# Optimization experiments

Hardware: AMD Instinct MI355X
Metric: run time of the kernel (lower is better)

## Reference

```python
import jax, jax.numpy as jnp
import numpy as np
from jax import lax

EPOCHS = 3
D_IN, D_OUT = 20, 18
_BN_EPS = 1e-5
_RECT_EPS = 1e-4


def _sym(a):
    return 0.5 * (a + jnp.swapaxes(a, -1, -2))


def _logm(a):
    s, u = jnp.linalg.eigh(_sym(a))
    return jnp.einsum('...ij,...j,...kj->...ik', u, jnp.log(s), u)


def _expm(a):
    s, u = jnp.linalg.eigh(_sym(a))
    return jnp.einsum('...ij,...j,...kj->...ik', u, jnp.exp(s), u)


def _rectify(a):
    # SPDRectified: clamp eigenvalues at epsilon
    s, u = jnp.linalg.eigh(_sym(a))
    s = jnp.maximum(s, _RECT_EPS)
    return jnp.einsum('...ij,...j,...kj->...ik', u, s, u)


def _bn(x, g, b):
    # training-mode BatchNorm2d (biased variance, as torch uses for normalization)
    m = x.mean(axis=(0, 2, 3), keepdims=True)
    v = x.var(axis=(0, 2, 3), keepdims=True)
    return (x - m) * lax.rsqrt(v + _BN_EPS) * g[None, :, None, None] + b[None, :, None, None]


def _patch_lens(n, epochs):
    base = n // epochs
    lens = [base] * epochs
    for i in range(n - base * epochs):
        lens[i] += 1
    return lens


def _forward(x, conv1_w, conv1_b, bn1_g, bn1_b, conv2_w, conv2_b, bn2_g, bn2_b,
             Wq, Wk, Wv, lin_w, lin_b):
    B = x.shape[0]
    # conv1: Conv2d(1, 22, (22, 1)) -- full contraction over the 22 EEG channels
    h = jnp.einsum('oh,bht->bot', conv1_w, x[:, 0]) + conv1_b[None, :, None]
    h = _bn(h[:, :, None, :], bn1_g, bn1_b)  # (B,22,1,T)
    # conv2: Conv2d(22, 20, (1, 12), padding=(0, 6)) -> time length T+1
    h = lax.conv_general_dilated(h, conv2_w, (1, 1), [(0, 0), (6, 6)],
                                 dimension_numbers=('NCHW', 'OIHW', 'NCHW'))
    h = h + conv2_b[None, :, None, None]
    h = _bn(h, bn2_g, bn2_b)
    sig = h[:, :, 0, :]  # (B, 20, T+1)
    # E2R: split time axis into EPOCHS patches, trace-normalized covariance per patch
    covs, off = [], 0
    eye = jnp.eye(D_IN, dtype=x.dtype)
    for L in _patch_lens(sig.shape[-1], EPOCHS):
        seg = sig[:, :, off:off + L]
        off += L
        seg = seg - seg.mean(axis=-1, keepdims=True)
        c = seg @ jnp.swapaxes(seg, -1, -2) / (L - 1)
        c = c / jnp.trace(c, axis1=-2, axis2=-1)[:, None, None]
        covs.append(c + 1e-5 * eye)
    cov = jnp.stack(covs, axis=1)  # (B, EPOCHS, 20, 20)
    # SPDTransform (bilinear congruence W^T X W) for Q, K, V
    Q = jnp.einsum('ia,bmij,jc->bmac', Wq, cov, Wq)
    K = jnp.einsum('ia,bmij,jc->bmac', Wk, cov, Wk)
    V = jnp.einsum('ia,bmij,jc->bmac', Wv, cov, Wv)
    logQ, logK, logV = _logm(Q), _logm(K), _logm(V)
    # log-Euclidean distance: sum of singular values of D D^T == ||D||_F^2
    # energy[b, i, j] = || logK[b,i] - logQ[b,j] ||_F^2 (matches the repeat/expand layout)
    diff = logK[:, :, None] - logQ[:, None, :]  # (B, m, m, d, d)
    energy = jnp.sum(diff * diff, axis=(-1, -2))  # (B, m, m)
    f = 1.0 / (1.0 + jnp.log1p(energy))
    prob = jax.nn.softmax(f, axis=-2)      # softmax over dim=-2 (the K index)
    prob = jnp.swapaxes(prob, -1, -2)      # permute(0, 2, 1)
    # LogEuclideanMean: weighted mean in log domain, then matrix exp
    mean_log = jnp.einsum('bpi,bikl->bpkl', prob, logV)
    out = _expm(mean_log)
    out = _rectify(out)
    tang = _logm(out)
    ri, ci = np.triu_indices(D_OUT)
    feat = tang[:, :, ri, ci].reshape(B, -1)  # (B, EPOCHS * 171)
    return feat @ lin_w.T + lin_b


def setup_inputs():
    key = jax.random.key(0)
    ks = jax.random.split(key, 16)
    B, C, T = 1024, 22, 438
    f32 = jnp.float32
    return {
        'x': jax.random.normal(ks[0], (B, 1, C, T), f32),
        'conv1_w': 0.1 * jax.random.normal(ks[1], (22, 22), f32),
        'conv1_b': 0.1 * jax.random.normal(ks[2], (22,), f32),
        'bn1_g': 1.0 + 0.1 * jax.random.normal(ks[3], (22,), f32),
        'bn1_b': 0.1 * jax.random.normal(ks[4], (22,), f32),
        'conv2_w': 0.05 * jax.random.normal(ks[5], (20, 22, 1, 12), f32),
        'conv2_b': 0.1 * jax.random.normal(ks[6], (20,), f32),
        'bn2_g': 1.0 + 0.1 * jax.random.normal(ks[7], (20,), f32),
        'bn2_b': 0.1 * jax.random.normal(ks[8], (20,), f32),
        'Wq': jnp.linalg.qr(jax.random.normal(ks[9], (20, 18), f32))[0],
        'Wk': jnp.linalg.qr(jax.random.normal(ks[10], (20, 18), f32))[0],
        'Wv': jnp.linalg.qr(jax.random.normal(ks[11], (20, 18), f32))[0],
        'lin_w': 0.05 * jax.random.normal(ks[12], (4, 9 * 19 * EPOCHS), f32),
        'lin_b': jnp.zeros((4,), f32),
    }


def reference(x, conv1_w, conv1_b, bn1_g, bn1_b, conv2_w, conv2_b, bn2_g, bn2_b,
              Wq, Wk, Wv, lin_w, lin_b):
    return _forward(x, conv1_w, conv1_b, bn1_g, bn1_b, conv2_w, conv2_b,
                    bn2_g, bn2_b, Wq, Wk, Wv, lin_w, lin_b)
```

## Files before the change

### kernel.cpp

```cpp
#include <hip/hip_runtime.h>
#include <cmath>

#define B_ 1024
#define CIN_ 22
#define T1_ 438
#define COUT_ 20
#define T2_ 439

#define OFF_S 0
#define OFF_M 32
#define OFF_SUM2 576
#define OFF_SSQ2 608
#define OFF_A2 640
#define OFF_ACC_END 704
#define OFF_C 1024
#define OFF_LQ (OFF_C + B_*3*400)
#define OFF_LK (OFF_LQ + B_*3*324)
#define OFF_LV (OFF_LK + B_*3*324)
#define OFF_WEFF (OFF_LV + B_*3*324)
#define OFF_BPRE (OFF_WEFF + 5280)

__global__ __launch_bounds__(256) void k_zero(float* ws){
  for(int i=threadIdx.x; i<OFF_ACC_END; i+=256) ws[i]=0.f;
}

__global__ __launch_bounds__(256) void k_moment(const float* __restrict__ x, float* __restrict__ ws){
  __shared__ float xs[CIN_][440];
  int b=blockIdx.x;
  const float* xb = x + (size_t)b*CIN_*T1_;
  for(int i=threadIdx.x;i<CIN_*T1_;i+=256){
    int h=i/T1_, t=i-h*T1_;
    xs[h][t]=xb[i];
  }
  if(threadIdx.x<CIN_){ xs[threadIdx.x][438]=0.f; xs[threadIdx.x][439]=0.f; }
  __syncthreads();
  for(int tgt=threadIdx.x; tgt<275; tgt+=256){
    if(tgt<253){
      int r=tgt, i=0;
      while(true){ int c=CIN_-i; if(r<c) break; r-=c; i++; }
      int j=i+r;
      const float4* ri=(const float4*)&xs[i][0];
      const float4* rj=(const float4*)&xs[j][0];
      float acc=0.f;
      for(int t=0;t<110;t++){
        float4 a=ri[t], bb=rj[t];
        acc += a.x*bb.x + a.y*bb.y + a.z*bb.z + a.w*bb.w;
      }
      atomicAdd(&ws[OFF_M + i*CIN_ + j], acc);
    } else {
      int c=tgt-253;
      const float4* rc=(const float4*)&xs[c][0];
      float acc=0.f;
      for(int t=0;t<110;t++){
        float4 a=rc[t];
        acc += a.x + a.y + a.z + a.w;
      }
      atomicAdd(&ws[OFF_S + c], acc);
    }
  }
}

__global__ __launch_bounds__(256) void k_prep(const float* __restrict__ w1, const float* __restrict__ cb1,
                                              const float* __restrict__ g1, const float* __restrict__ bb1,
                                              const float* __restrict__ w2, float* __restrict__ ws){
  __shared__ float a1s[CIN_], e1s[CIN_];
  int tid=threadIdx.x;
  if(tid<CIN_){
    int c=tid;
    const double N = (double)B_*T1_;
    double wS=0.0, wMw=0.0;
    for(int h=0;h<CIN_;h++) wS += (double)w1[c*CIN_+h]*(double)ws[OFF_S+h];
    for(int h=0;h<CIN_;h++){
      for(int h2=0;h2<CIN_;h2++){
        int i=h<h2?h:h2, j=h<h2?h2:h;
        wMw += (double)w1[c*CIN_+h]*(double)w1[c*CIN_+h2]*(double)ws[OFF_M+i*CIN_+j];
      }
    }
    double bc=cb1[c];
    double mean=wS/N+bc;
    double ex2=(wMw+2.0*bc*wS)/N+bc*bc;
    double var=ex2-mean*mean;
    double a1=(double)g1[c]/sqrt(var+1e-5);
    double d1=(double)bb1[c]-mean*a1;
    a1s[c]=(float)a1;
    e1s[c]=(float)(a1*bc+d1);
  }
  __syncthreads();
  for(int idx=tid; idx<5280; idx+=256){
    int o=idx/264, r=idx-o*264, h=r/12, k=r-h*12;
    float s=0.f;
    for(int i=0;i<CIN_;i++) s += w2[(o*CIN_+i)*12+k]*a1s[i]*w1[i*CIN_+h];
    ws[OFF_WEFF+idx]=s;
  }
  if(tid<COUT_){
    float pre=0.f;
    ws[OFF_BPRE+tid*13+0]=0.f;
    for(int k=0;k<12;k++){
      float wb=0.f;
      for(int i=0;i<CIN_;i++) wb += w2[(tid*CIN_+i)*12+k]*e1s[i];
      pre += wb;
      ws[OFF_BPRE+tid*13+k+1]=pre;
    }
  }
}

__global__ __launch_bounds__(256) void k_cov(const float* __restrict__ x,
                                             float* __restrict__ ws){
  __shared__ float Wl[5280];
  __shared__ float preL[COUT_][13];
  __shared__ float xs[CIN_][168];
  __shared__ float h2w[COUT_][156];
  __shared__ float pmu[COUT_];
  int b=blockIdx.x, tid=threadIdx.x;
  for(int i=tid;i<5280;i+=256) Wl[i]=ws[OFF_WEFF+i];
  for(int i=tid;i<260;i+=256) ((float*)preL)[i]=ws[OFF_BPRE+i];
  int pi=0,pj=0;
  if(tid<210){ int r=tid,i=0; while(true){int c=COUT_-i; if(r<c)break; r-=c; i++;} pi=i; pj=i+r; }
  int sc = tid-210;
  float ac1=0.f, ac2=0.f;
  const float* xb = x + (size_t)b*CIN_*T1_;
  int o = tid/12, cch = tid-12*o;
  int t0 = cch*13;
  for(int p=0;p<3;p++){
    const int off = (p==0)?0:((p==1)?147:293);
    const int L = (p==0)?147:146;
    __syncthreads();
    for(int idx=tid; idx<CIN_*168; idx+=256){
      int h=idx/168, c2=idx-h*168;
      int gxt = off-6+c2;
      xs[h][c2] = (c2<167 && gxt>=0 && gxt<T1_) ? xb[h*T1_+gxt] : 0.f;
    }
    __syncthreads();
    if(tid<240){
      float acc[13];
      #pragma unroll
      for(int j=0;j<13;j++){
        int gt = off+t0+j;
        int kmin = 6-gt; kmin = kmin<0?0:kmin;
        int kmax = 443-gt; kmax = kmax>11?11:kmax;
        acc[j] = (kmax>=kmin)? preL[o][kmax+1]-preL[o][kmin] : 0.f;
      }
      const float* Wo = &Wl[o*264];
      for(int h=0;h<CIN_;h++){
        float xw[24];
        #pragma unroll
        for(int c2=0;c2<24;c2++) xw[c2]=xs[h][t0+c2];
        const float* Wh = Wo + h*12;
        #pragma unroll
        for(int k=0;k<12;k++){
          float w=Wh[k];
          #pragma unroll
          for(int j=0;j<13;j++) acc[j] += w*xw[j+k];
        }
      }
      #pragma unroll
      for(int j=0;j<13;j++) if(t0+j<L) h2w[o][t0+j]=acc[j];
    } else {
      int npad = 156-L;
      for(int z=tid-240; z<COUT_*npad; z+=16){
        int oo=z/npad, c2=z-oo*npad;
        h2w[oo][L+c2]=0.f;
      }
    }
    __syncthreads();
    float s=0.f;
    if(tid<210){
      const float4* ri=(const float4*)&h2w[pi][0];
      const float4* rj=(const float4*)&h2w[pj][0];
      for(int t=0;t<39;t++){
        float4 a=ri[t], bb=rj[t];
        s += a.x*bb.x + a.y*bb.y + a.z*bb.z + a.w*bb.w;
      }
    } else if(sc>=0 && sc<COUT_){
      const float4* rc=(const float4*)&h2w[sc][0];
      float s1=0.f,s2=0.f;
      for(int t=0;t<39;t++){
        float4 a=rc[t];
        s1 += a.x+a.y+a.z+a.w;
        s2 += a.x*a.x+a.y*a.y+a.z*a.z+a.w*a.w;
      }
      ac1+=s1; ac2+=s2; pmu[sc]=s1/(float)L;
    }
    __syncthreads();
    if(tid<210){
      s -= (float)L*pmu[pi]*pmu[pj];
      float* Cb = ws + OFF_C + ((size_t)b*3+p)*400;
      Cb[pi*COUT_+pj]=s; Cb[pj*COUT_+pi]=s;
    }
  }
  if(sc>=0 && sc<COUT_){
    atomicAdd(&ws[OFF_SUM2+sc], ac1);
    atomicAdd(&ws[OFF_SSQ2+sc], ac2);
  }
}

__global__ void k_fin2(const float* __restrict__ g2, float* __restrict__ ws){
  int c=threadIdx.x; if(c>=COUT_) return;
  const double N=(double)B_*T2_;
  double m=ws[OFF_SUM2+c]/N;
  double v=ws[OFF_SSQ2+c]/N - m*m;
  ws[OFF_A2+c]=(float)((double)g2[c]/sqrt(v+1e-5));
}

__device__ __forceinline__ void bl_jacobi18(float own[18], float &dgo,
                                            int l18, int gb, bool act, int maxsweep){
  int self = gb + l18;
  for(int sweep=0; sweep<maxsweep; sweep++){
    { float d0=0.f,d1=0.f;
      #pragma unroll
      for(int k=0;k<18;k+=2){ d0+=own[k]*own[k]; d1+=own[k+1]*own[k+1]; }
      dgo=d0+d1;
    }
    float smax=0.f;
    for(int r=0;r<17;r++){
      int t = 2*r - l18;
      t += (t<0)?17:0;
      t -= (t>=17)?17:0;
      int pa = (l18==17)? r : ((t==l18)?17:t);
      int src = act ? (gb + pa) : self;
      float oth[18];
      #pragma unroll
      for(int k=0;k<18;k++) oth[k]=__shfl(own[k], src);
      float dgx = __shfl(dgo, src);
      float a0=0.f,a1=0.f;
      #pragma unroll
      for(int k=0;k<18;k+=2){ a0+=own[k]*oth[k]; a1+=own[k+1]*oth[k+1]; }
      float apq=a0+a1;
      bool isP = l18 < pa;
      float dgp = isP? dgo : dgx;
      float dgq = isP? dgx : dgo;
      float tau = __fdividef(dgq-dgp, 2.f*apq);
      float tt  = __fdividef(copysignf(1.f,tau), fabsf(tau)+sqrtf(1.f+tau*tau));
      float c   = rsqrtf(1.f+tt*tt);
      float s   = tt*c;
      bool  z   = (apq==0.f) || !act;
      tt=z?0.f:tt; c=z?1.f:c; s=z?0.f:s;
      smax=fmaxf(smax,fabsf(s));
      float sgn = isP ? -s : s;
      #pragma unroll
      for(int k=0;k<18;k++) own[k] = c*own[k] + sgn*oth[k];
      dgo = isP ? (dgp - tt*apq) : (dgq + tt*apq);
    }
    if(__all(smax<3e-3f)) break;
  }
  float d0=0.f,d1=0.f;
  #pragma unroll
  for(int k=0;k<18;k+=2){ d0+=own[k]*own[k]; d1+=own[k+1]*own[k+1]; }
  dgo=d0+d1;
}

__global__ __launch_bounds__(64) void k_eigh3(const float* __restrict__ Wq,
                                              const float* __restrict__ Wk,
                                              const float* __restrict__ Wv,
                                              float* __restrict__ ws){
  __shared__ float S[2933];
  float* Wa  = S;
  float* a2s = S+1080;
  float* Cs  = S+1100;
  float* Tt  = S+1500;
  float* ob  = S+1878;
  float* gl  = S+2850;
  float* trp = S+2904;
  int bp=blockIdx.x, tid=threadIdx.x;
  int g=tid/18, l18=tid-18*g;
  bool act = (g<3);
  int gb = g*18;

  if(tid<20) a2s[tid]=ws[OFF_A2+tid];
  __syncthreads();
  for(int i=tid;i<1080;i+=64){
    int m=i/360, r=i-m*360, row=r/18;
    const float* W=(m==0)?Wq:((m==1)?Wk:Wv);
    Wa[i]=W[r]*a2s[row];
  }
  const float* Cb=ws+OFF_C+(size_t)bp*400;
  for(int i=tid;i<400;i+=64) Cs[i]=Cb[i];
  __syncthreads();
  if(tid==0){
    float tr=0.f;
    #pragma unroll
    for(int i=0;i<20;i++) tr += Cs[i*20+i]*a2s[i]*a2s[i];
    trp[0]=tr;
  }
  __syncthreads();
  float tr=trp[0];
  float sh=1e-5f*tr;
  float logtr=logf(tr);
  for(int m=0;m<3;m++){
    const float* Wm=Wa+m*360;
    for(int idx=tid; idx<360; idx+=64){
      int a=idx/20, j=idx-a*20;
      float s=0.f;
      for(int i=0;i<20;i++) s += Wm[i*18+a]*Cs[i*20+j];
      Tt[a*21+j]=s;
    }
    __syncthreads();
    for(int idx=tid; idx<324; idx+=64){
      int a=idx/18, c=idx-a*18;
      float s=0.f;
      for(int j=0;j<20;j++) s += Tt[a*21+j]*Wm[j*18+c];
      ob[m*324+idx]=s;
    }
    __syncthreads();
  }
  float own[18], dgo=0.f;
  if(act){
    const float* Ag=ob+g*324;
    #pragma unroll
    for(int k=0;k<18;k++)
      own[k]=0.5f*(Ag[k*18+l18]+Ag[l18*18+k]) + ((k==l18)?sh:0.f);
  } else {
    #pragma unroll
    for(int k=0;k<18;k++) own[k]=0.f;
  }
  __syncthreads();
  bl_jacobi18(own,dgo,l18,gb,act,8);
  float dp=fmaxf(dgo,1e-30f);
  float gv=__fdividef(0.5f*logf(dp)-logtr, dp);
  float* Mc = Wa;
  if(act){
    #pragma unroll
    for(int k=0;k<18;k++) Mc[g*342 + k*19 + l18]=own[k];
    gl[g*18+l18]=gv;
  }
  __syncthreads();
  if(tid<54){
    int mat=tid/18, i=tid-mat*18;
    float w[18];
    #pragma unroll
    for(int k=0;k<18;k++) w[k]=gl[mat*18+k]*Mc[mat*342+i*19+k];
    for(int j=0;j<18;j++){
      float s=0.f;
      #pragma unroll
      for(int k=0;k<18;k++) s += w[k]*Mc[mat*342+j*19+k];
      ob[mat*324+i*18+j]=s;
    }
  }
  __syncthreads();
  const float4* s4=(const float4*)ob;
  for(int i=tid;i<243;i+=64){
    int mat=i/81, r=i-mat*81;
    float4* dst=(float4*)(ws + ((mat==0)?OFF_LQ:((mat==1)?OFF_LK:OFF_LV)) + (size_t)bp*324);
    dst[r]=s4[i];
  }
}

__global__ __launch_bounds__(64) void k_att2(const float* __restrict__ lw,
                                             const float* __restrict__ lb,
                                             float* __restrict__ ws,
                                             float* __restrict__ out){
  __shared__ float lv[972];
  __shared__ float lqk[1944];
  __shared__ float e9[9];
  __shared__ float prob[9];
  __shared__ float Mc[1026];
  __shared__ float gl[54];
  int b=blockIdx.x, tid=threadIdx.x;
  const float4* LQ4=(const float4*)(ws+OFF_LQ+(size_t)b*972);
  const float4* LK4=(const float4*)(ws+OFF_LK+(size_t)b*972);
  const float4* LV4=(const float4*)(ws+OFF_LV+(size_t)b*972);
  float4* lqk4=(float4*)lqk; float4* lv4=(float4*)lv;
  for(int i=tid;i<243;i+=64){ lqk4[i]=LQ4[i]; lqk4[243+i]=LK4[i]; lv4[i]=LV4[i]; }
  __syncthreads();
  if(tid<36){
    int d=tid>>2, sub=tid&3;
    int ii=d/3, p=d-ii*3;
    const float* kk=lqk+972+ii*324+sub*81;
    const float* qq=lqk+p*324+sub*81;
    float s=0.f;
    for(int el=0;el<81;el++){ float dd=kk[el]-qq[el]; s+=dd*dd; }
    s += __shfl_xor(s,1); s += __shfl_xor(s,2);
    if(sub==0) e9[d]=s;
  }
  __syncthreads();
  if(tid<3){
    int p=tid;
    float f0=1.f/(1.f+log1pf(e9[0+p]));
    float f1=1.f/(1.f+log1pf(e9[3+p]));
    float f2=1.f/(1.f+log1pf(e9[6+p]));
    float mx=fmaxf(f0,fmaxf(f1,f2));
    float x0=expf(f0-mx), x1=expf(f1-mx), x2=expf(f2-mx);
    float inv=1.f/(x0+x1+x2);
    prob[p*3+0]=x0*inv; prob[p*3+1]=x1*inv; prob[p*3+2]=x2*inv;
  }
  __syncthreads();
  float* ml = lqk;
  for(int idx=tid; idx<972; idx+=64){
    int p=idx/324, el=idx-p*324;
    ml[idx]=prob[p*3+0]*lv[el]+prob[p*3+1]*lv[324+el]+prob[p*3+2]*lv[648+el];
  }
  __syncthreads();
  int g=tid/18, l18=tid-18*g;
  bool act=(g<3);
  int gb=g*18;
  float own[18], dgo=0.f;
  if(act){
    const float* Ag=ml+g*324;
    #pragma unroll
    for(int k=0;k<18;k++)
      own[k]=0.5f*(Ag[k*18+l18]+Ag[l18*18+k]) + ((k==l18)?12.f:0.f);
  } else {
    #pragma unroll
    for(int k=0;k<18;k++) own[k]=0.f;
  }
  __syncthreads();
  bl_jacobi18(own,dgo,l18,gb,act,8);
  float lam=sqrtf(fmaxf(dgo,1e-12f));
  float gv=__fdividef(fmaxf(lam-12.f,-9.2103404f), fmaxf(dgo,1e-12f));
  if(act){
    #pragma unroll
    for(int k=0;k<18;k++) Mc[g*342 + k*19 + l18]=own[k];
    gl[g*18+l18]=gv;
  }
  __syncthreads();
  float* feat = lv;
  if(tid<54){
    int mat=tid/18, i=tid-mat*18;
    float w[18];
    #pragma unroll
    for(int k=0;k<18;k++) w[k]=gl[mat*18+k]*Mc[mat*342+i*19+k];
    int base = mat*171 + (i*18 - (i*(i-1))/2) - i;
    for(int j=i;j<18;j++){
      float s=0.f;
      #pragma unroll
      for(int k=0;k<18;k++) s += w[k]*Mc[mat*342+j*19+k];
      feat[base+j]=s;
    }
  }
  __syncthreads();
  int j4 = tid&3, chunk = tid>>2;
  float s=0.f;
  const float* wj = lw + j4*513;
  for(int k=chunk; k<513; k+=16) s += feat[k]*wj[k];
  s += __shfl_xor(s,4); s += __shfl_xor(s,8);
  s += __shfl_xor(s,16); s += __shfl_xor(s,32);
  if(chunk==0) out[b*4+j4] = s + lb[j4];
}

extern "C" void kernel_launch(void* const* d_in, const int* in_sizes, int n_in,
                              void* d_out, int out_size, void* d_ws, size_t ws_size,
                              hipStream_t stream){
  const float* x  =(const float*)d_in[0];
  const float* w1 =(const float*)d_in[1];
  const float* cb1=(const float*)d_in[2];
  const float* g1 =(const float*)d_in[3];
  const float* bb1=(const float*)d_in[4];
  const float* w2 =(const float*)d_in[5];
  const float* g2 =(const float*)d_in[7];
  const float* Wq =(const float*)d_in[9];
  const float* Wk =(const float*)d_in[10];
  const float* Wv =(const float*)d_in[11];
  const float* lw =(const float*)d_in[12];
  const float* lb =(const float*)d_in[13];
  float* ws=(float*)d_ws;
  float* out=(float*)d_out;

  k_zero<<<1,256,0,stream>>>(ws);
  k_moment<<<B_,256,0,stream>>>(x,ws);
  k_prep<<<1,256,0,stream>>>(w1,cb1,g1,bb1,w2,ws);
  k_cov<<<B_,256,0,stream>>>(x,ws);
  k_fin2<<<1,64,0,stream>>>(g2,ws);
  k_eigh3<<<3072,64,0,stream>>>(Wq,Wk,Wv,ws);
  k_att2<<<B_,64,0,stream>>>(lw,lb,ws,out);
}
```

Before: 406.3 us.

## Fuse per-epoch log-eigh and attention kernels into one 192-thread block per sample

Merges the per-(sample,epoch) eigendecomposition kernel and the per-sample attention kernel into one kernel with three wavefronts per sample, one per epoch. The log-mapped Q/K/V matrices stay in shared memory instead of round-tripping through the global workspace, and one launch is removed. The cost is a larger shared-memory footprint per block, and the second-stage Jacobi runs only 18 of 64 lanes in each wave, so occupancy and lane utilisation may drop.

After: 429.1 us, median of 2. +5.6%, slower.

```diff
diff --git a/kernel.cpp b/kernel.cpp
--- a/kernel.cpp
+++ b/kernel.cpp
@@ -14,10 +14,7 @@
 #define OFF_A2 640
 #define OFF_ACC_END 704
 #define OFF_C 1024
-#define OFF_LQ (OFF_C + B_*3*400)
-#define OFF_LK (OFF_LQ + B_*3*324)
-#define OFF_LV (OFF_LK + B_*3*324)
-#define OFF_WEFF (OFF_LV + B_*3*324)
+#define OFF_WEFF (OFF_C + B_*3*400)
 #define OFF_BPRE (OFF_WEFF + 5280)
 
 __global__ __launch_bounds__(256) void k_zero(float* ws){
@@ -249,63 +246,77 @@
   dgo=d0+d1;
 }
 
-__global__ __launch_bounds__(64) void k_eigh3(const float* __restrict__ Wq,
-                                              const float* __restrict__ Wk,
-                                              const float* __restrict__ Wv,
-                                              float* __restrict__ ws){
-  __shared__ float S[2933];
-  float* Wa  = S;
-  float* a2s = S+1080;
-  float* Cs  = S+1100;
-  float* Tt  = S+1500;
-  float* ob  = S+1878;
-  float* gl  = S+2850;
-  float* trp = S+2904;
-  int bp=blockIdx.x, tid=threadIdx.x;
-  int g=tid/18, l18=tid-18*g;
-  bool act = (g<3);
-  int gb = g*18;
-
-  if(tid<20) a2s[tid]=ws[OFF_A2+tid];
-  __syncthreads();
-  for(int i=tid;i<1080;i+=64){
+#define F_A2S 0
+#define F_WA 20
+#define F_CS 1100
+#define F_TT 2300
+#define F_TRS 3434
+#define F_LTR 3437
+#define F_LG 3440
+#define F_E9 6356
+#define F_PROB 6365
+#define F_SC 20
+#define F_GL1 3098
+#define F_ML 20
+#define F_MC2 992
+#define F_GL2 2018
+#define F_FEAT 3440
+
+__global__ __launch_bounds__(192) void k_fused(const float* __restrict__ Wq,
+                                               const float* __restrict__ Wk,
+                                               const float* __restrict__ Wv,
+                                               const float* __restrict__ lw,
+                                               const float* __restrict__ lb,
+                                               float* __restrict__ ws,
+                                               float* __restrict__ out){
+  __shared__ float S[6374];
+  int b=blockIdx.x, tid=threadIdx.x;
+  int w=tid>>6, wl=tid&63;
+  if(tid<20) S[F_A2S+tid]=ws[OFF_A2+tid];
+  __syncthreads();
+  for(int i=tid;i<1080;i+=192){
     int m=i/360, r=i-m*360, row=r/18;
     const float* W=(m==0)?Wq:((m==1)?Wk:Wv);
-    Wa[i]=W[r]*a2s[row];
-  }
-  const float* Cb=ws+OFF_C+(size_t)bp*400;
-  for(int i=tid;i<400;i+=64) Cs[i]=Cb[i];
-  __syncthreads();
-  if(tid==0){
+    S[F_WA+i]=W[r]*S[F_A2S+row];
+  }
+  {
+    const float* Cb=ws+OFF_C+((size_t)b*3+w)*400;
+    for(int i=wl;i<400;i+=64) S[F_CS+w*400+i]=Cb[i];
+  }
+  if(wl==0){
     float tr=0.f;
     #pragma unroll
-    for(int i=0;i<20;i++) tr += Cs[i*20+i]*a2s[i]*a2s[i];
-    trp[0]=tr;
-  }
-  __syncthreads();
-  float tr=trp[0];
-  float sh=1e-5f*tr;
-  float logtr=logf(tr);
+    for(int i=0;i<20;i++) tr += S[F_CS+w*400+i*20+i]*S[F_A2S+i]*S[F_A2S+i];
+    S[F_TRS+w]=tr;
+    S[F_LTR+w]=logf(tr);
+  }
+  __syncthreads();
   for(int m=0;m<3;m++){
-    const float* Wm=Wa+m*360;
-    for(int idx=tid; idx<360; idx+=64){
+    const float* Wm=S+F_WA+m*360;
+    const float* Cw=S+F_CS+w*400;
+    float* Tw=S+F_TT+w*378;
+    for(int idx=wl; idx<360; idx+=64){
       int a=idx/20, j=idx-a*20;
       float s=0.f;
-      for(int i=0;i<20;i++) s += Wm[i*18+a]*Cs[i*20+j];
-      Tt[a*21+j]=s;
-    }
-    __syncthreads();
-    for(int idx=tid; idx<324; idx+=64){
+      for(int i=0;i<20;i++) s += Wm[i*18+a]*Cw[i*20+j];
+      Tw[a*21+j]=s;
+    }
+    __syncthreads();
+    for(int idx=wl; idx<324; idx+=64){
       int a=idx/18, c=idx-a*18;
       float s=0.f;
-      for(int j=0;j<20;j++) s += Tt[a*21+j]*Wm[j*18+c];
-      ob[m*324+idx]=s;
-    }
-    __syncthreads();
-  }
+      for(int j=0;j<20;j++) s += Tw[a*21+j]*Wm[j*18+c];
+      S[F_LG + m*972 + w*324 + idx]=s;
+    }
+    __syncthreads();
+  }
+  int g=wl/18, l18=wl-18*g;
+  bool act=(g<3);
+  float tr_w=S[F_TRS+w], ltr_w=S[F_LTR+w];
+  float sh=1e-5f*tr_w;
   float own[18], dgo=0.f;
   if(act){
-    const float* Ag=ob+g*324;
+    const float* Ag=S+F_LG+g*972+w*324;
     #pragma unroll
     for(int k=0;k<18;k++)
       own[k]=0.5f*(Ag[k*18+l18]+Ag[l18*18+k]) + ((k==l18)?sh:0.f);
@@ -314,127 +325,101 @@
     for(int k=0;k<18;k++) own[k]=0.f;
   }
   __syncthreads();
-  bl_jacobi18(own,dgo,l18,gb,act,8);
+  bl_jacobi18(own,dgo,l18,g*18,act,8);
   float dp=fmaxf(dgo,1e-30f);
-  float gv=__fdividef(0.5f*logf(dp)-logtr, dp);
-  float* Mc = Wa;
+  float gv=__fdividef(0.5f*logf(dp)-ltr_w, dp);
+  float* Mc1=S+F_SC+w*1026;
+  float* gl1=S+F_GL1+w*54;
   if(act){
     #pragma unroll
-    for(int k=0;k<18;k++) Mc[g*342 + k*19 + l18]=own[k];
-    gl[g*18+l18]=gv;
-  }
-  __syncthreads();
-  if(tid<54){
-    int mat=tid/18, i=tid-mat*18;
-    float w[18];
-    #pragma unroll
-    for(int k=0;k<18;k++) w[k]=gl[mat*18+k]*Mc[mat*342+i*19+k];
+    for(int k=0;k<18;k++) Mc1[g*342 + k*19 + l18]=own[k];
+    gl1[g*18+l18]=gv;
+  }
+  if(wl<54){
+    int mat=g, i=l18;
+    float w18[18];
+    #pragma unroll
+    for(int k=0;k<18;k++) w18[k]=gl1[mat*18+k]*Mc1[mat*342+i*19+k];
+    float* ob=S+F_LG+mat*972+w*324+i*18;
     for(int j=0;j<18;j++){
       float s=0.f;
       #pragma unroll
-      for(int k=0;k<18;k++) s += w[k]*Mc[mat*342+j*19+k];
-      ob[mat*324+i*18+j]=s;
-    }
-  }
-  __syncthreads();
-  const float4* s4=(const float4*)ob;
-  for(int i=tid;i<243;i+=64){
-    int mat=i/81, r=i-mat*81;
-    float4* dst=(float4*)(ws + ((mat==0)?OFF_LQ:((mat==1)?OFF_LK:OFF_LV)) + (size_t)bp*324);
-    dst[r]=s4[i];
-  }
-}
-
-__global__ __launch_bounds__(64) void k_att2(const float* __restrict__ lw,
-                                             const float* __restrict__ lb,
-                                             float* __restrict__ ws,
-                                             float* __restrict__ out){
-  __shared__ float lv[972];
-  __shared__ float lqk[1944];
-  __shared__ float e9[9];
-  __shared__ float prob[9];
-  __shared__ float Mc[1026];
-  __shared__ float gl[54];
-  int b=blockIdx.x, tid=threadIdx.x;
-  const float4* LQ4=(const float4*)(ws+OFF_LQ+(size_t)b*972);
-  const float4* LK4=(const float4*)(ws+OFF_LK+(size_t)b*972);
-  const float4* LV4=(const float4*)(ws+OFF_LV+(size_t)b*972);
-  float4* lqk4=(float4*)lqk; float4* lv4=(float4*)lv;
-  for(int i=tid;i<243;i+=64){ lqk4[i]=LQ4[i]; lqk4[243+i]=LK4[i]; lv4[i]=LV4[i]; }
+      for(int k=0;k<18;k++) s += w18[k]*Mc1[mat*342+j*19+k];
+      ob[j]=s;
+    }
+  }
   __syncthreads();
   if(tid<36){
     int d=tid>>2, sub=tid&3;
     int ii=d/3, p=d-ii*3;
-    const float* kk=lqk+972+ii*324+sub*81;
-    const float* qq=lqk+p*324+sub*81;
+    const float* kk=S+F_LG+972+ii*324+sub*81;
+    const float* qq=S+F_LG+p*324+sub*81;
     float s=0.f;
     for(int el=0;el<81;el++){ float dd=kk[el]-qq[el]; s+=dd*dd; }
     s += __shfl_xor(s,1); s += __shfl_xor(s,2);
-    if(sub==0) e9[d]=s;
+    if(sub==0) S[F_E9+d]=s;
   }
   __syncthreads();
   if(tid<3){
     int p=tid;
-    float f0=1.f/(1.f+log1pf(e9[0+p]));
-    float f1=1.f/(1.f+log1pf(e9[3+p]));
-    float f2=1.f/(1.f+log1pf(e9[6+p]));
+    float f0=1.f/(1.f+log1pf(S[F_E9+0+p]));
+    float f1=1.f/(1.f+log1pf(S[F_E9+3+p]));
+    float f2=1.f/(1.f+log1pf(S[F_E9+6+p]));
     float mx=fmaxf(f0,fmaxf(f1,f2));
     float x0=expf(f0-mx), x1=expf(f1-mx), x2=expf(f2-mx);
     float inv=1.f/(x0+x1+x2);
-    prob[p*3+0]=x0*inv; prob[p*3+1]=x1*inv; prob[p*3+2]=x2*inv;
-  }
-  __syncthreads();
-  float* ml = lqk;
-  for(int idx=tid; idx<972; idx+=64){
+    S[F_PROB+p*3+0]=x0*inv; S[F_PROB+p*3+1]=x1*inv; S[F_PROB+p*3+2]=x2*inv;
+  }
+  __syncthreads();
+  for(int idx=tid; idx<972; idx+=192){
     int p=idx/324, el=idx-p*324;
-    ml[idx]=prob[p*3+0]*lv[el]+prob[p*3+1]*lv[324+el]+prob[p*3+2]*lv[648+el];
-  }
-  __syncthreads();
-  int g=tid/18, l18=tid-18*g;
-  bool act=(g<3);
-  int gb=g*18;
-  float own[18], dgo=0.f;
-  if(act){
-    const float* Ag=ml+g*324;
+    const float* LV=S+F_LG+1944;
+    S[F_ML+idx]=S[F_PROB+p*3+0]*LV[el]+S[F_PROB+p*3+1]*LV[324+el]+S[F_PROB+p*3+2]*LV[648+el];
+  }
+  __syncthreads();
+  bool act2=(wl<18);
+  float own2[18], dgo2=0.f;
+  if(act2){
+    const float* Ag=S+F_ML+w*324;
     #pragma unroll
     for(int k=0;k<18;k++)
-      own[k]=0.5f*(Ag[k*18+l18]+Ag[l18*18+k]) + ((k==l18)?12.f:0.f);
+      own2[k]=0.5f*(Ag[k*18+wl]+Ag[wl*18+k]) + ((k==wl)?12.f:0.f);
   } else {
     #pragma unroll
-    for(int k=0;k<18;k++) own[k]=0.f;
-  }
-  __syncthreads();
-  bl_jacobi18(own,dgo,l18,gb,act,8);
-  float lam=sqrtf(fmaxf(dgo,1e-12f));
-  float gv=__fdividef(fmaxf(lam-12.f,-9.2103404f), fmaxf(dgo,1e-12f));
-  if(act){
-    #pragma unroll
-    for(int k=0;k<18;k++) Mc[g*342 + k*19 + l18]=own[k];
-    gl[g*18+l18]=gv;
-  }
-  __syncthreads();
-  float* feat = lv;
+    for(int k=0;k<18;k++) own2[k]=0.f;
+  }
+  bl_jacobi18(own2,dgo2,wl,0,act2,8);
+  float lam=sqrtf(fmaxf(dgo2,1e-12f));
+  float gv2=__fdividef(fmaxf(lam-12.f,-9.2103404f), fmaxf(dgo2,1e-12f));
+  if(act2){
+    #pragma unroll
+    for(int k=0;k<18;k++) S[F_MC2 + w*342 + k*19 + wl]=own2[k];
+    S[F_GL2 + w*18 + wl]=gv2;
+  }
+  __syncthreads();
   if(tid<54){
     int mat=tid/18, i=tid-mat*18;
-    float w[18];
-    #pragma unroll
-    for(int k=0;k<18;k++) w[k]=gl[mat*18+k]*Mc[mat*342+i*19+k];
+    float w18[18];
+    #pragma unroll
+    for(int k=0;k<18;k++) w18[k]=S[F_GL2+mat*18+k]*S[F_MC2+mat*342+i*19+k];
     int base = mat*171 + (i*18 - (i*(i-1))/2) - i;
     for(int j=i;j<18;j++){
       float s=0.f;
       #pragma unroll
-      for(int k=0;k<18;k++) s += w[k]*Mc[mat*342+j*19+k];
-      feat[base+j]=s;
-    }
-  }
-  __syncthreads();
-  int j4 = tid&3, chunk = tid>>2;
-  float s=0.f;
-  const float* wj = lw + j4*513;
-  for(int k=chunk; k<513; k+=16) s += feat[k]*wj[k];
-  s += __shfl_xor(s,4); s += __shfl_xor(s,8);
-  s += __shfl_xor(s,16); s += __shfl_xor(s,32);
-  if(chunk==0) out[b*4+j4] = s + lb[j4];
+      for(int k=0;k<18;k++) s += w18[k]*S[F_MC2+mat*342+j*19+k];
+      S[F_FEAT+base+j]=s;
+    }
+  }
+  __syncthreads();
+  if(tid<64){
+    int j4 = tid&3, chunk = tid>>2;
+    float s=0.f;
+    const float* wj = lw + j4*513;
+    for(int k=chunk; k<513; k+=16) s += S[F_FEAT+k]*wj[k];
+    s += __shfl_xor(s,4); s += __shfl_xor(s,8);
+    s += __shfl_xor(s,16); s += __shfl_xor(s,32);
+    if(chunk==0) out[b*4+j4] = s + lb[j4];
+  }
 }
 
 extern "C" void kernel_launch(void* const* d_in, const int* in_sizes, int n_in,
@@ -460,6 +445,5 @@
   k_prep<<<1,256,0,stream>>>(w1,cb1,g1,bb1,w2,ws);
   k_cov<<<B_,256,0,stream>>>(x,ws);
   k_fin2<<<1,64,0,stream>>>(g2,ws);
-  k_eigh3<<<3072,64,0,stream>>>(Wq,Wk,Wv,ws);
-  k_att2<<<B_,64,0,stream>>>(lw,lb,ws,out);
-}
+  k_fused<<<B_,192,0,stream>>>(Wq,Wk,Wv,lw,lb,ws,out);
+}
```
